# Kernel tuning notes

Hardware: AMD Instinct MI355X
Metric: run time of the kernel (lower is better)

Reference implementation:

```python
import jax, jax.numpy as jnp
import numpy as np

G, B, S, D = 4, 1, 1024, 2048   # num_gpus (chunks), batch, seq_local, model dim
H, DH = 32, 64                  # heads, dim_head; inner_dim = H*DH = D
EPS = 1e-6
NEG = -1e30                     # finite stand-in for -inf lse init (grad-safe)


def setup_inputs() -> dict:
    key = jax.random.key(0)
    ks = jax.random.split(key, 8)
    wsc = 1.0 / np.sqrt(D)  # keep pre-softmax logits in a sane range
    return {
        'x':  jax.random.normal(ks[0], (G, B, S, D), jnp.float32),
        'Wq': jax.random.normal(ks[1], (D, D), jnp.float32) * wsc,
        'bq': jnp.zeros((D,), jnp.float32),
        'Wk': jax.random.normal(ks[2], (D, D), jnp.float32) * wsc,
        'bk': jnp.zeros((D,), jnp.float32),
        'Wv': jax.random.normal(ks[3], (D, D), jnp.float32) * wsc,
        'bv': jnp.zeros((D,), jnp.float32),
        'qn_w': jnp.ones((D,), jnp.float32),
        'kn_w': jnp.ones((D,), jnp.float32),
        'Wo': jax.random.normal(ks[4], (D, D), jnp.float32) * wsc,
        'bo': jnp.zeros((D,), jnp.float32),
    }


def _rms_norm(t, w):
    return t * jax.lax.rsqrt(jnp.mean(t * t, axis=-1, keepdims=True) + EPS) * w


def reference(x, Wq, bq, Wk, bk, Wv, bv, qn_w, kn_w, Wo, bo):
    # x: [G, B, S, D] -- per-'GPU' sequence chunks
    q = _rms_norm(x @ Wq.T + bq, qn_w)
    k = _rms_norm(x @ Wk.T + bk, kn_w)
    v = x @ Wv.T + bv
    split = lambda t: t.reshape(G, B, S, H, DH).transpose(0, 1, 3, 2, 4)  # [G,B,H,S,DH]
    q, k, v = split(q), split(k), split(v)
    scale = 1.0 / np.sqrt(DH)

    out = jnp.zeros_like(q)
    lse = jnp.full((G, B, H, S, 1), NEG, q.dtype)
    kc, vc = k, v
    # Ring: each chunk attends to the visiting K/V chunk with online softmax.
    for _ in range(G):
        scores = jnp.einsum('gbhqd,gbhkd->gbhqk', q, kc) * scale
        m = scores.max(axis=-1, keepdims=True)
        e = jnp.exp(scores - m)
        ssum = e.sum(axis=-1, keepdims=True)
        chunk_lse = m + jnp.log(ssum)
        chunk_out = jnp.einsum('gbhqk,gbhkd->gbhqd', e / ssum, vc)
        new_lse = jnp.logaddexp(lse, chunk_lse)
        out = out * jnp.exp(lse - new_lse) + chunk_out * jnp.exp(chunk_lse - new_lse)
        lse = new_lse
        # rotate K/V around the ring: device i receives from device i-1
        kc = jnp.roll(kc, 1, axis=0)
        vc = jnp.roll(vc, 1, axis=0)

    o = out.transpose(0, 1, 3, 2, 4).reshape(G, B, S, H * DH)
    return o @ Wo.T + bo
```

## Files before the change

### kernel.cpp

```cpp
#include <hip/hip_runtime.h>

typedef __bf16 bf16x8 __attribute__((ext_vector_type(8)));
typedef float f32x4 __attribute__((ext_vector_type(4)));
typedef float f32x16 __attribute__((ext_vector_type(16)));
typedef unsigned short u16x8 __attribute__((ext_vector_type(8)));
typedef unsigned u32x2 __attribute__((ext_vector_type(2)));
typedef unsigned u32x4 __attribute__((ext_vector_type(4)));

__device__ __forceinline__ unsigned short f2bf(float f) {
  union { float f; unsigned u; } v; v.f = f;
  unsigned r = (v.u + 0x7fffu + ((v.u >> 16) & 1u)) >> 16;
  return (unsigned short)r;
}
__device__ __forceinline__ float bf2f(unsigned short s) {
  union { unsigned u; float f; } v; v.u = ((unsigned)s) << 16;
  return v.f;
}

#define GLD16(g, l)                                                        \
  __builtin_amdgcn_global_load_lds(                                        \
      (const __attribute__((address_space(1))) void*)(g),                  \
      (__attribute__((address_space(3))) void*)(l), 16, 0, 0)

__device__ __forceinline__ int swzc(int row, int colel) {
  return colel ^ ((((row & 7) ^ ((row >> 3) & 7)) & 7) << 3);
}

__device__ __forceinline__ u32x2 plswap(unsigned a, unsigned b) {
  return __builtin_amdgcn_permlane32_swap(a, b, false, false);
}
__device__ __forceinline__ float pair_sum(float x) {
  u32x2 r = plswap(__float_as_uint(x), __float_as_uint(x));
  return __uint_as_float(r.x) + __uint_as_float(r.y);
}
__device__ __forceinline__ unsigned cvtpk(float a, float b) {
  unsigned r;
  asm("v_cvt_pk_bf16_f32 %0, %1, %2" : "=v"(r) : "v"(a), "v"(b));
  return r;
}

__global__ __launch_bounds__(256) void cast_all_kernel(
    const float* __restrict__ x,
    const float* __restrict__ w0, const float* __restrict__ w1,
    const float* __restrict__ w2, const float* __restrict__ w3,
    unsigned short* __restrict__ xo,
    unsigned short* __restrict__ o0, unsigned short* __restrict__ o1,
    unsigned short* __restrict__ o2, unsigned short* __restrict__ o3) {
  int i = blockIdx.x * 256 + threadIdx.x;
  int stride = gridDim.x * 256;
  for (; i < 6291456; i += stride) {
    const float* src;
    unsigned short* dst;
    int j;
    if (i < 2097152) {
      src = x; dst = xo; j = i;
    } else {
      int k = i - 2097152;
      int sel = k >> 20;
      src = sel == 0 ? w0 : sel == 1 ? w1 : sel == 2 ? w2 : w3;
      dst = sel == 0 ? o0 : sel == 1 ? o1 : sel == 2 ? o2 : o3;
      j = k & 1048575;
    }
    float4 f = reinterpret_cast<const float4*>(src)[j];
    ushort4 s;
    s.x = f2bf(f.x); s.y = f2bf(f.y); s.z = f2bf(f.z); s.w = f2bf(f.w);
    reinterpret_cast<ushort4*>(dst)[j] = s;
  }
}


#define STG_A(STEP, KS, BUF)                                                   \
  GLD16(Ag + (size_t)(row0 + st_row0) * 2048 + (STEP) * 64 + (KS) * 32 +       \
            st_col0,                                                           \
        &ls[((BUF) * 2 + (KS)) * 4096 + (wid * 2) * 512]);                     \
  GLD16(Ag + (size_t)(row0 + st_row1) * 2048 + (STEP) * 64 + (KS) * 32 +       \
            st_col1,                                                           \
        &ls[((BUF) * 2 + (KS)) * 4096 + (wid * 2 + 1) * 512]);

#define STG_B(STEP, KS, BUF)                                                   \
  GLD16(Bg + (size_t)(col0 + st_row0) * 2048 + (STEP) * 64 + (KS) * 32 +       \
            st_col0,                                                           \
        &ls[16384 + ((BUF) * 2 + (KS)) * 4096 + (wid * 2) * 512]);             \
  GLD16(Bg + (size_t)(col0 + st_row1) * 2048 + (STEP) * 64 + (KS) * 32 +       \
            st_col1,                                                           \
        &ls[16384 + ((BUF) * 2 + (KS)) * 4096 + (wid * 2 + 1) * 512]);

#define VM8 asm volatile("s_waitcnt vmcnt(8)" ::: "memory");
#define VM4 asm volatile("s_waitcnt vmcnt(4)" ::: "memory");
#define VM0 asm volatile("s_waitcnt vmcnt(0)" ::: "memory");

#define PHASE4(BUF, KS, STG, VMW)                                              \
  {                                                                            \
    const int pb = ((BUF) * 2 + (KS)) * 4096;                                  \
    bf16x8 af0 = *(const bf16x8*)&ls[pb + offA[0]];                            \
    bf16x8 af1 = *(const bf16x8*)&ls[pb + offA[1]];                            \
    bf16x8 af2 = *(const bf16x8*)&ls[pb + offA[2]];                            \
    bf16x8 af3 = *(const bf16x8*)&ls[pb + offA[3]];                            \
    bf16x8 bf0 = *(const bf16x8*)&ls[16384 + pb + offB[0]];                    \
    bf16x8 bf1 = *(const bf16x8*)&ls[16384 + pb + offB[1]];                    \
    bf16x8 bf2 = *(const bf16x8*)&ls[16384 + pb + offB[2]];                    \
    bf16x8 bf3 = *(const bf16x8*)&ls[16384 + pb + offB[3]];                    \
    STG;                                                                       \
    __builtin_amdgcn_s_barrier();                                              \
    __builtin_amdgcn_s_setprio(1);                                             \
    acc[0][0] = __builtin_amdgcn_mfma_f32_16x16x32_bf16(af0, bf0, acc[0][0], 0, 0, 0); \
    acc[0][1] = __builtin_amdgcn_mfma_f32_16x16x32_bf16(af0, bf1, acc[0][1], 0, 0, 0); \
    acc[0][2] = __builtin_amdgcn_mfma_f32_16x16x32_bf16(af0, bf2, acc[0][2], 0, 0, 0); \
    acc[0][3] = __builtin_amdgcn_mfma_f32_16x16x32_bf16(af0, bf3, acc[0][3], 0, 0, 0); \
    acc[1][0] = __builtin_amdgcn_mfma_f32_16x16x32_bf16(af1, bf0, acc[1][0], 0, 0, 0); \
    acc[1][1] = __builtin_amdgcn_mfma_f32_16x16x32_bf16(af1, bf1, acc[1][1], 0, 0, 0); \
    acc[1][2] = __builtin_amdgcn_mfma_f32_16x16x32_bf16(af1, bf2, acc[1][2], 0, 0, 0); \
    acc[1][3] = __builtin_amdgcn_mfma_f32_16x16x32_bf16(af1, bf3, acc[1][3], 0, 0, 0); \
    acc[2][0] = __builtin_amdgcn_mfma_f32_16x16x32_bf16(af2, bf0, acc[2][0], 0, 0, 0); \
    acc[2][1] = __builtin_amdgcn_mfma_f32_16x16x32_bf16(af2, bf1, acc[2][1], 0, 0, 0); \
    acc[2][2] = __builtin_amdgcn_mfma_f32_16x16x32_bf16(af2, bf2, acc[2][2], 0, 0, 0); \
    acc[2][3] = __builtin_amdgcn_mfma_f32_16x16x32_bf16(af2, bf3, acc[2][3], 0, 0, 0); \
    acc[3][0] = __builtin_amdgcn_mfma_f32_16x16x32_bf16(af3, bf0, acc[3][0], 0, 0, 0); \
    acc[3][1] = __builtin_amdgcn_mfma_f32_16x16x32_bf16(af3, bf1, acc[3][1], 0, 0, 0); \
    acc[3][2] = __builtin_amdgcn_mfma_f32_16x16x32_bf16(af3, bf2, acc[3][2], 0, 0, 0); \
    acc[3][3] = __builtin_amdgcn_mfma_f32_16x16x32_bf16(af3, bf3, acc[3][3], 0, 0, 0); \
    __builtin_amdgcn_s_setprio(0);                                             \
    VMW;                                                                       \
    __builtin_amdgcn_s_barrier();                                              \
  }

template <int F32OUT>
__global__ __launch_bounds__(256, 2) void gemm4p(
    const unsigned short* __restrict__ Ag,
    const unsigned short* __restrict__ W0, const unsigned short* __restrict__ W1,
    const unsigned short* __restrict__ W2,
    const float* __restrict__ b0, const float* __restrict__ b1,
    const float* __restrict__ b2,
    void* __restrict__ C0, void* __restrict__ C1, void* __restrict__ C2) {
  extern __shared__ __align__(16) unsigned short ls[];

  const int lin = blockIdx.y * gridDim.x + blockIdx.x;
  const int cpx = (gridDim.x * gridDim.y) >> 3;
  const int swz = (lin & 7) * cpx + (lin >> 3);
  const int bx = swz % gridDim.x, by = swz / gridDim.x;

  const int gcol = bx * 128;
  const int sel = gcol >> 11;
  const unsigned short* Bg = sel == 0 ? W0 : sel == 1 ? W1 : W2;
  const float* bias = sel == 0 ? b0 : sel == 1 ? b1 : b2;
  void* Cp = sel == 0 ? C0 : sel == 1 ? C1 : C2;
  const int col0 = gcol & 2047;
  const int row0 = by * 128;

  const int tid = threadIdx.x, lane = tid & 63, wid = tid >> 6;
  const int l15 = lane & 15, l4 = lane >> 4;
  const int wm = wid >> 1, wn = wid & 1;

  const int ci0 = wid * 2, ci1 = wid * 2 + 1;
  const int st_row0 = ci0 * 16 + (lane >> 2);
  const int st_row1 = ci1 * 16 + (lane >> 2);
  const int sl2a = ((lane >> 2) & 3) ^ ((lane >> 4) & 3);
  const int st_col0 = (((lane & 3) ^ (sl2a ^ (ci0 & 3))) * 8);
  const int st_col1 = (((lane & 3) ^ (sl2a ^ (ci1 & 3))) * 8);

  const int lsel = (l15 & 3) ^ ((l15 >> 2) & 3);
  int offA[4], offB[4];
#pragma unroll
  for (int f = 0; f < 4; ++f)
    offA[f] = (wm * 64 + f * 16 + l15) * 32 + ((l4 ^ lsel ^ (f & 3)) & 3) * 8;
#pragma unroll
  for (int ni = 0; ni < 4; ++ni)
    offB[ni] =
        (wn * 64 + ni * 16 + l15) * 32 + ((l4 ^ lsel ^ ((wn * 4 + ni) & 3)) & 3) * 8;

  f32x4 acc[4][4] = {};

  STG_A(0, 0, 0); STG_B(0, 0, 0);
  STG_A(0, 1, 0); STG_B(0, 1, 0);
  STG_A(1, 0, 1); STG_B(1, 0, 1);
  VM8;
  __builtin_amdgcn_s_barrier();

  for (int it = 0; it < 15; ++it) {
    const int sE = 2 * it, sO = sE + 1;
    PHASE4(0, 0, STG_A(sO, 1, 1) STG_B(sO, 1, 1), VM8);
    PHASE4(0, 1, STG_A(sE + 2, 0, 0) STG_B(sE + 2, 0, 0), VM8);
    PHASE4(1, 0, STG_A(sE + 2, 1, 0) STG_B(sE + 2, 1, 0), VM8);
    PHASE4(1, 1, STG_A(sO + 2, 0, 1) STG_B(sO + 2, 0, 1), VM8);
  }
  PHASE4(0, 0, STG_A(31, 1, 1) STG_B(31, 1, 1), VM8);
  PHASE4(0, 1, , VM4);
  PHASE4(1, 0, , VM0);
  PHASE4(1, 1, , );

#pragma unroll
  for (int f = 0; f < 4; ++f)
#pragma unroll
    for (int ni = 0; ni < 4; ++ni)
#pragma unroll
      for (int r = 0; r < 4; ++r) {
        int row = row0 + wm * 64 + f * 16 + l4 * 4 + r;
        int col = col0 + wn * 64 + ni * 16 + l15;
        float v = acc[f][ni][r] + bias[col];
        if (F32OUT)
          ((float*)Cp)[(size_t)row * 2048 + col] = v;
        else
          ((unsigned short*)Cp)[(size_t)row * 2048 + col] = f2bf(v);
      }
}

__global__ __launch_bounds__(256) void rmsnorm2_kernel(
    unsigned short* __restrict__ Qb, unsigned short* __restrict__ Kb,
    const float* __restrict__ qw, const float* __restrict__ kw) {
  const int row = blockIdx.x;
  unsigned short* p;
  const float* w;
  if (row < 4096) { p = Qb + (size_t)row * 2048; w = qw; }
  else            { p = Kb + (size_t)(row - 4096) * 2048; w = kw; }
  const int tid = threadIdx.x;
  u16x8 v = *(const u16x8*)&p[tid * 8];
  float f[8];
  float ss = 0.f;
#pragma unroll
  for (int j = 0; j < 8; ++j) { f[j] = bf2f(v[j]); ss += f[j] * f[j]; }
#pragma unroll
  for (int m = 1; m < 64; m <<= 1) ss += __shfl_xor(ss, m, 64);
  __shared__ float red[4];
  const int wid = tid >> 6, lane = tid & 63;
  if (lane == 0) red[wid] = ss;
  __syncthreads();
  float tot = red[0] + red[1] + red[2] + red[3];
  float rs = rsqrtf(tot * (1.0f / 2048.0f) + 1e-6f);
  u16x8 o;
#pragma unroll
  for (int j = 0; j < 8; ++j) o[j] = f2bf(f[j] * rs * w[tid * 8 + j]);
  *(u16x8*)&p[tid * 8] = o;
}

__global__ __launch_bounds__(256, 2) void flash_attn(
    const unsigned short* __restrict__ Q, const unsigned short* __restrict__ K,
    const unsigned short* __restrict__ V, unsigned short* __restrict__ O) {
  __shared__ unsigned short Ks[2][64 * 64];
  __shared__ unsigned short Vs[2][64 * 64];
  const int bid = blockIdx.x;
  const int sw = (bid & 7) * 64 + (bid >> 3);
  const int h = sw >> 4;
  const int q0 = (sw & 15) * 256;
  const int tid = threadIdx.x, lane = tid & 63, wid = tid >> 6;
  const int l31 = lane & 31, hi = lane >> 5;

  const int kr0 = wid * 16 + (lane >> 3);
  const int kc0 = (lane & 7) * 8;
  const int vkey = (tid & 31) * 2;
  const int vd0 = (tid >> 5) * 8;

  const float QSCALE = 0.125f * 1.44269504f;
  bf16x8 qf0[4], qf1[4];
  {
    const int qr0 = q0 + wid * 64 + l31;
#pragma unroll
    for (int kt = 0; kt < 4; ++kt) {
      bf16x8 r0 = *(const bf16x8*)&Q[(size_t)qr0 * 2048 + h * 64 + kt * 16 + hi * 8];
      bf16x8 r1 = *(const bf16x8*)&Q[(size_t)(qr0 + 32) * 2048 + h * 64 + kt * 16 + hi * 8];
#pragma unroll
      for (int j = 0; j < 8; ++j) {
        qf0[kt][j] = (__bf16)((float)r0[j] * QSCALE);
        qf1[kt][j] = (__bf16)((float)r1[j] * QSCALE);
      }
    }
  }

  int off[2][4];
#pragma unroll
  for (int kb = 0; kb < 2; ++kb) {
    const int row = kb * 32 + l31;
    const int sl = (((row & 7) ^ ((row >> 3) & 7)) & 7) << 3;
#pragma unroll
    for (int kt = 0; kt < 4; ++kt)
      off[kb][kt] = row * 64 + ((kt * 16 + hi * 8) ^ sl);
  }

  float l0 = 0.f, l1 = 0.f;
  f32x16 oa0[2] = {}, oa1[2] = {};

  u16x8 kreg0, kreg1, vreg0, vreg1;
  auto loadKV = [&](int kt0) {
    kreg0 = *(const u16x8*)&K[(size_t)(kt0 + kr0) * 2048 + h * 64 + kc0];
    kreg1 = *(const u16x8*)&K[(size_t)(kt0 + kr0 + 8) * 2048 + h * 64 + kc0];
    vreg0 = *(const u16x8*)&V[(size_t)(kt0 + vkey) * 2048 + h * 64 + vd0];
    vreg1 = *(const u16x8*)&V[(size_t)(kt0 + vkey + 1) * 2048 + h * 64 + vd0];
  };
  auto writeKV = [&](int b) {
    *(u16x8*)&Ks[b][kr0 * 64 + swzc(kr0, kc0)] = kreg0;
    *(u16x8*)&Ks[b][(kr0 + 8) * 64 + swzc(kr0 + 8, kc0)] = kreg1;
#pragma unroll
    for (int d = 0; d < 8; ++d) {
      int row = vd0 + d;
      *(unsigned*)&Vs[b][row * 64 + swzc(row, vkey)] =
          (unsigned)vreg0[d] | ((unsigned)vreg1[d] << 16);
    }
  };

  loadKV(0);
  writeKV(0);
  __syncthreads();

  for (int t = 0; t < 64; ++t) {
    const int cur = t & 1;
    if (t < 63) loadKV((t + 1) * 64);

    const unsigned short* Kc = Ks[cur];
    const unsigned short* Vc = Vs[cur];

    bf16x8 kf[2][4];
#pragma unroll
    for (int kb = 0; kb < 2; ++kb)
#pragma unroll
      for (int kt = 0; kt < 4; ++kt)
        kf[kb][kt] = *(const bf16x8*)&Kc[off[kb][kt]];

    f32x16 st0[2], st1[2];
    __builtin_amdgcn_s_setprio(1);
#pragma unroll
    for (int kb = 0; kb < 2; ++kb) {
      f32x16 a = {};
#pragma unroll
      for (int kt = 0; kt < 4; ++kt)
        a = __builtin_amdgcn_mfma_f32_32x32x16_bf16(kf[kb][kt], qf0[kt], a, 0, 0, 0);
      st0[kb] = a;
    }
#pragma unroll
    for (int kb = 0; kb < 2; ++kb) {
      f32x16 a = {};
#pragma unroll
      for (int kt = 0; kt < 4; ++kt)
        a = __builtin_amdgcn_mfma_f32_32x32x16_bf16(kf[kb][kt], qf1[kt], a, 0, 0, 0);
      st1[kb] = a;
    }
    __builtin_amdgcn_s_setprio(0);

    unsigned pk0[16], pk1[16];
    {
      float s0 = 0.f, s1 = 0.f, s2 = 0.f, s3 = 0.f;
#pragma unroll
      for (int kb = 0; kb < 2; ++kb)
#pragma unroll
        for (int j = 0; j < 8; ++j) {
          float pa = __builtin_amdgcn_exp2f(st0[kb][2 * j]);
          float pb = __builtin_amdgcn_exp2f(st0[kb][2 * j + 1]);
          if ((j & 3) == 0) s0 += pa + pb;
          else if ((j & 3) == 1) s1 += pa + pb;
          else if ((j & 3) == 2) s2 += pa + pb;
          else s3 += pa + pb;
          pk0[kb * 8 + j] = cvtpk(pa, pb);
        }
      l0 += (s0 + s1) + (s2 + s3);
    }
    {
      float s0 = 0.f, s1 = 0.f, s2 = 0.f, s3 = 0.f;
#pragma unroll
      for (int kb = 0; kb < 2; ++kb)
#pragma unroll
        for (int j = 0; j < 8; ++j) {
          float pa = __builtin_amdgcn_exp2f(st1[kb][2 * j]);
          float pb = __builtin_amdgcn_exp2f(st1[kb][2 * j + 1]);
          if ((j & 3) == 0) s0 += pa + pb;
          else if ((j & 3) == 1) s1 += pa + pb;
          else if ((j & 3) == 2) s2 += pa + pb;
          else s3 += pa + pb;
          pk1[kb * 8 + j] = cvtpk(pa, pb);
        }
      l1 += (s0 + s1) + (s2 + s3);
    }

    bf16x8 pfrag0[4], pfrag1[4];
#pragma unroll
    for (int kt = 0; kt < 4; ++kt) {
      u32x2 sa = plswap(pk0[4 * kt + 0], pk0[4 * kt + 2]);
      u32x2 sb = plswap(pk0[4 * kt + 1], pk0[4 * kt + 3]);
      union { u32x4 u; bf16x8 b; } w;
      w.u.x = sa.x; w.u.y = sb.x; w.u.z = sa.y; w.u.w = sb.y;
      pfrag0[kt] = w.b;
      u32x2 sc = plswap(pk1[4 * kt + 0], pk1[4 * kt + 2]);
      u32x2 sd = plswap(pk1[4 * kt + 1], pk1[4 * kt + 3]);
      union { u32x4 u; bf16x8 b; } w2;
      w2.u.x = sc.x; w2.u.y = sd.x; w2.u.z = sc.y; w2.u.w = sd.y;
      pfrag1[kt] = w2.b;
    }

    __builtin_amdgcn_s_setprio(1);
#pragma unroll
    for (int dv = 0; dv < 2; ++dv) {
      bf16x8 vf[4];
#pragma unroll
      for (int kt = 0; kt < 4; ++kt)
        vf[kt] = *(const bf16x8*)&Vc[off[dv][kt]];
#pragma unroll
      for (int kt = 0; kt < 4; ++kt)
        oa0[dv] = __builtin_amdgcn_mfma_f32_32x32x16_bf16(vf[kt], pfrag0[kt], oa0[dv], 0, 0, 0);
#pragma unroll
      for (int kt = 0; kt < 4; ++kt)
        oa1[dv] = __builtin_amdgcn_mfma_f32_32x32x16_bf16(vf[kt], pfrag1[kt], oa1[dv], 0, 0, 0);
    }
    __builtin_amdgcn_s_setprio(0);

    if (t < 63) {
      writeKV(cur ^ 1);
      __syncthreads();
    }
  }

  const float inv0 = 1.0f / pair_sum(l0);
  const float inv1 = 1.0f / pair_sum(l1);
  const int qr0 = q0 + wid * 64 + l31;
#pragma unroll
  for (int dv = 0; dv < 2; ++dv)
#pragma unroll
    for (int tq = 0; tq < 4; ++tq) {
      int dh = 32 * dv + 8 * tq + 4 * hi;
      unsigned a0 = cvtpk(oa0[dv][4 * tq + 0] * inv0, oa0[dv][4 * tq + 1] * inv0);
      unsigned a1 = cvtpk(oa0[dv][4 * tq + 2] * inv0, oa0[dv][4 * tq + 3] * inv0);
      u32x2 wa = {a0, a1};
      *(u32x2*)&O[(size_t)qr0 * 2048 + h * 64 + dh] = wa;
      unsigned b0 = cvtpk(oa1[dv][4 * tq + 0] * inv1, oa1[dv][4 * tq + 1] * inv1);
      unsigned b1 = cvtpk(oa1[dv][4 * tq + 2] * inv1, oa1[dv][4 * tq + 3] * inv1);
      u32x2 wb = {b0, b1};
      *(u32x2*)&O[(size_t)(qr0 + 32) * 2048 + h * 64 + dh] = wb;
    }
}

extern "C" void kernel_launch(void* const* d_in, const int* in_sizes, int n_in,
                              void* d_out, int out_size, void* d_ws, size_t ws_size,
                              hipStream_t stream) {
  const float* x  = (const float*)d_in[0];
  const float* Wq = (const float*)d_in[1];
  const float* bq = (const float*)d_in[2];
  const float* Wk = (const float*)d_in[3];
  const float* bk = (const float*)d_in[4];
  const float* Wv = (const float*)d_in[5];
  const float* bv = (const float*)d_in[6];
  const float* qn = (const float*)d_in[7];
  const float* kn = (const float*)d_in[8];
  const float* Wo = (const float*)d_in[9];
  const float* bo = (const float*)d_in[10];

  char* w = (char*)d_ws;
  unsigned short* Xbf = (unsigned short*)(w);
  unsigned short* Wqb = (unsigned short*)(w + 16777216);
  unsigned short* Wkb = (unsigned short*)(w + 25165824);
  unsigned short* Wvb = (unsigned short*)(w + 33554432);
  unsigned short* Wob = (unsigned short*)(w + 41943040);
  unsigned short* Qb  = (unsigned short*)(w + 50331648);
  unsigned short* Kb  = (unsigned short*)(w + 67108864);
  unsigned short* Vb  = (unsigned short*)(w + 83886080);
  unsigned short* Ob  = Xbf;

  cast_all_kernel<<<3072, 256, 0, stream>>>(x, Wq, Wk, Wv, Wo,
                                            Xbf, Wqb, Wkb, Wvb, Wob);

  gemm4p<0><<<dim3(48, 32), 256, 65536, stream>>>(
      Xbf, Wqb, Wkb, Wvb, bq, bk, bv, Qb, Kb, Vb);

  rmsnorm2_kernel<<<8192, 256, 0, stream>>>(Qb, Kb, qn, kn);

  flash_attn<<<512, 256, 0, stream>>>(Qb, Kb, Vb, Ob);

  gemm4p<1><<<dim3(16, 32), 256, 65536, stream>>>(
      Ob, Wob, Wob, Wob, bo, bo, bo, d_out, d_out, d_out);
}
```

Before: 362.4 us.

## Enlarge GEMM tile to 256x128 with 512 threads and 4-stage K pipeline

```diff
diff --git a/kernel.cpp b/kernel.cpp
--- a/kernel.cpp
+++ b/kernel.cpp
@@ -69,70 +69,64 @@
 }
 
 
-#define STG_A(STEP, KS, BUF)                                                   \
-  GLD16(Ag + (size_t)(row0 + st_row0) * 2048 + (STEP) * 64 + (KS) * 32 +       \
-            st_col0,                                                           \
-        &ls[((BUF) * 2 + (KS)) * 4096 + (wid * 2) * 512]);                     \
-  GLD16(Ag + (size_t)(row0 + st_row1) * 2048 + (STEP) * 64 + (KS) * 32 +       \
-            st_col1,                                                           \
-        &ls[((BUF) * 2 + (KS)) * 4096 + (wid * 2 + 1) * 512]);
-
-#define STG_B(STEP, KS, BUF)                                                   \
-  GLD16(Bg + (size_t)(col0 + st_row0) * 2048 + (STEP) * 64 + (KS) * 32 +       \
-            st_col0,                                                           \
-        &ls[16384 + ((BUF) * 2 + (KS)) * 4096 + (wid * 2) * 512]);             \
-  GLD16(Bg + (size_t)(col0 + st_row1) * 2048 + (STEP) * 64 + (KS) * 32 +       \
-            st_col1,                                                           \
-        &ls[16384 + ((BUF) * 2 + (KS)) * 4096 + (wid * 2 + 1) * 512]);
-
-#define VM8 asm volatile("s_waitcnt vmcnt(8)" ::: "memory");
-#define VM4 asm volatile("s_waitcnt vmcnt(4)" ::: "memory");
+#define SGA(SLICE, SLOT)                                                       \
+  GLD16(Ag + (size_t)(row0 + ar0) * 2048 + (SLICE) * 32 + ac0,                 \
+        &As[SLOT][ci0 * 512]);                                                 \
+  GLD16(Ag + (size_t)(row0 + ar1) * 2048 + (SLICE) * 32 + ac1,                 \
+        &As[SLOT][ci1 * 512]);
+
+#define SGB(SLICE, SLOT)                                                       \
+  GLD16(Bg + (size_t)(col0 + br0) * 2048 + (SLICE) * 32 + bc0,                 \
+        &Bs[SLOT][wid * 512]);
+
+#define VM6 asm volatile("s_waitcnt vmcnt(6)" ::: "memory");
+#define VM3 asm volatile("s_waitcnt vmcnt(3)" ::: "memory");
 #define VM0 asm volatile("s_waitcnt vmcnt(0)" ::: "memory");
 
-#define PHASE4(BUF, KS, STG, VMW)                                              \
+#define PH256(SLOT, STG, VMW)                                                  \
   {                                                                            \
-    const int pb = ((BUF) * 2 + (KS)) * 4096;                                  \
-    bf16x8 af0 = *(const bf16x8*)&ls[pb + offA[0]];                            \
-    bf16x8 af1 = *(const bf16x8*)&ls[pb + offA[1]];                            \
-    bf16x8 af2 = *(const bf16x8*)&ls[pb + offA[2]];                            \
-    bf16x8 af3 = *(const bf16x8*)&ls[pb + offA[3]];                            \
-    bf16x8 bf0 = *(const bf16x8*)&ls[16384 + pb + offB[0]];                    \
-    bf16x8 bf1 = *(const bf16x8*)&ls[16384 + pb + offB[1]];                    \
-    bf16x8 bf2 = *(const bf16x8*)&ls[16384 + pb + offB[2]];                    \
-    bf16x8 bf3 = *(const bf16x8*)&ls[16384 + pb + offB[3]];                    \
+    bf16x8 a0 = *(const bf16x8*)&As[SLOT][offA[0]];                            \
+    bf16x8 a1 = *(const bf16x8*)&As[SLOT][offA[1]];                            \
+    bf16x8 a2 = *(const bf16x8*)&As[SLOT][offA[2]];                            \
+    bf16x8 a3 = *(const bf16x8*)&As[SLOT][offA[3]];                            \
+    bf16x8 b0 = *(const bf16x8*)&Bs[SLOT][offB[0]];                            \
+    bf16x8 b1 = *(const bf16x8*)&Bs[SLOT][offB[1]];                            \
+    bf16x8 b2 = *(const bf16x8*)&Bs[SLOT][offB[2]];                            \
+    bf16x8 b3 = *(const bf16x8*)&Bs[SLOT][offB[3]];                            \
     STG;                                                                       \
     __builtin_amdgcn_s_barrier();                                              \
     __builtin_amdgcn_s_setprio(1);                                             \
-    acc[0][0] = __builtin_amdgcn_mfma_f32_16x16x32_bf16(af0, bf0, acc[0][0], 0, 0, 0); \
-    acc[0][1] = __builtin_amdgcn_mfma_f32_16x16x32_bf16(af0, bf1, acc[0][1], 0, 0, 0); \
-    acc[0][2] = __builtin_amdgcn_mfma_f32_16x16x32_bf16(af0, bf2, acc[0][2], 0, 0, 0); \
-    acc[0][3] = __builtin_amdgcn_mfma_f32_16x16x32_bf16(af0, bf3, acc[0][3], 0, 0, 0); \
-    acc[1][0] = __builtin_amdgcn_mfma_f32_16x16x32_bf16(af1, bf0, acc[1][0], 0, 0, 0); \
-    acc[1][1] = __builtin_amdgcn_mfma_f32_16x16x32_bf16(af1, bf1, acc[1][1], 0, 0, 0); \
-    acc[1][2] = __builtin_amdgcn_mfma_f32_16x16x32_bf16(af1, bf2, acc[1][2], 0, 0, 0); \
-    acc[1][3] = __builtin_amdgcn_mfma_f32_16x16x32_bf16(af1, bf3, acc[1][3], 0, 0, 0); \
-    acc[2][0] = __builtin_amdgcn_mfma_f32_16x16x32_bf16(af2, bf0, acc[2][0], 0, 0, 0); \
-    acc[2][1] = __builtin_amdgcn_mfma_f32_16x16x32_bf16(af2, bf1, acc[2][1], 0, 0, 0); \
-    acc[2][2] = __builtin_amdgcn_mfma_f32_16x16x32_bf16(af2, bf2, acc[2][2], 0, 0, 0); \
-    acc[2][3] = __builtin_amdgcn_mfma_f32_16x16x32_bf16(af2, bf3, acc[2][3], 0, 0, 0); \
-    acc[3][0] = __builtin_amdgcn_mfma_f32_16x16x32_bf16(af3, bf0, acc[3][0], 0, 0, 0); \
-    acc[3][1] = __builtin_amdgcn_mfma_f32_16x16x32_bf16(af3, bf1, acc[3][1], 0, 0, 0); \
-    acc[3][2] = __builtin_amdgcn_mfma_f32_16x16x32_bf16(af3, bf2, acc[3][2], 0, 0, 0); \
-    acc[3][3] = __builtin_amdgcn_mfma_f32_16x16x32_bf16(af3, bf3, acc[3][3], 0, 0, 0); \
+    acc[0][0] = __builtin_amdgcn_mfma_f32_16x16x32_bf16(a0, b0, acc[0][0], 0, 0, 0); \
+    acc[0][1] = __builtin_amdgcn_mfma_f32_16x16x32_bf16(a0, b1, acc[0][1], 0, 0, 0); \
+    acc[0][2] = __builtin_amdgcn_mfma_f32_16x16x32_bf16(a0, b2, acc[0][2], 0, 0, 0); \
+    acc[0][3] = __builtin_amdgcn_mfma_f32_16x16x32_bf16(a0, b3, acc[0][3], 0, 0, 0); \
+    acc[1][0] = __builtin_amdgcn_mfma_f32_16x16x32_bf16(a1, b0, acc[1][0], 0, 0, 0); \
+    acc[1][1] = __builtin_amdgcn_mfma_f32_16x16x32_bf16(a1, b1, acc[1][1], 0, 0, 0); \
+    acc[1][2] = __builtin_amdgcn_mfma_f32_16x16x32_bf16(a1, b2, acc[1][2], 0, 0, 0); \
+    acc[1][3] = __builtin_amdgcn_mfma_f32_16x16x32_bf16(a1, b3, acc[1][3], 0, 0, 0); \
+    acc[2][0] = __builtin_amdgcn_mfma_f32_16x16x32_bf16(a2, b0, acc[2][0], 0, 0, 0); \
+    acc[2][1] = __builtin_amdgcn_mfma_f32_16x16x32_bf16(a2, b1, acc[2][1], 0, 0, 0); \
+    acc[2][2] = __builtin_amdgcn_mfma_f32_16x16x32_bf16(a2, b2, acc[2][2], 0, 0, 0); \
+    acc[2][3] = __builtin_amdgcn_mfma_f32_16x16x32_bf16(a2, b3, acc[2][3], 0, 0, 0); \
+    acc[3][0] = __builtin_amdgcn_mfma_f32_16x16x32_bf16(a3, b0, acc[3][0], 0, 0, 0); \
+    acc[3][1] = __builtin_amdgcn_mfma_f32_16x16x32_bf16(a3, b1, acc[3][1], 0, 0, 0); \
+    acc[3][2] = __builtin_amdgcn_mfma_f32_16x16x32_bf16(a3, b2, acc[3][2], 0, 0, 0); \
+    acc[3][3] = __builtin_amdgcn_mfma_f32_16x16x32_bf16(a3, b3, acc[3][3], 0, 0, 0); \
     __builtin_amdgcn_s_setprio(0);                                             \
     VMW;                                                                       \
     __builtin_amdgcn_s_barrier();                                              \
   }
 
 template <int F32OUT>
-__global__ __launch_bounds__(256, 2) void gemm4p(
+__global__ __launch_bounds__(512, 2) void gemm256(
     const unsigned short* __restrict__ Ag,
     const unsigned short* __restrict__ W0, const unsigned short* __restrict__ W1,
     const unsigned short* __restrict__ W2,
     const float* __restrict__ b0, const float* __restrict__ b1,
     const float* __restrict__ b2,
     void* __restrict__ C0, void* __restrict__ C1, void* __restrict__ C2) {
-  extern __shared__ __align__(16) unsigned short ls[];
+  __shared__ unsigned short As[4][8192];
+  __shared__ unsigned short Bs[4][4096];
 
   const int lin = blockIdx.y * gridDim.x + blockIdx.x;
   const int cpx = (gridDim.x * gridDim.y) >> 3;
@@ -145,48 +139,49 @@
   const float* bias = sel == 0 ? b0 : sel == 1 ? b1 : b2;
   void* Cp = sel == 0 ? C0 : sel == 1 ? C1 : C2;
   const int col0 = gcol & 2047;
-  const int row0 = by * 128;
+  const int row0 = by * 256;
 
   const int tid = threadIdx.x, lane = tid & 63, wid = tid >> 6;
   const int l15 = lane & 15, l4 = lane >> 4;
   const int wm = wid >> 1, wn = wid & 1;
 
+  const int sl2a = ((lane >> 2) & 3) ^ ((lane >> 4) & 3);
   const int ci0 = wid * 2, ci1 = wid * 2 + 1;
-  const int st_row0 = ci0 * 16 + (lane >> 2);
-  const int st_row1 = ci1 * 16 + (lane >> 2);
-  const int sl2a = ((lane >> 2) & 3) ^ ((lane >> 4) & 3);
-  const int st_col0 = (((lane & 3) ^ (sl2a ^ (ci0 & 3))) * 8);
-  const int st_col1 = (((lane & 3) ^ (sl2a ^ (ci1 & 3))) * 8);
+  const int ar0 = ci0 * 16 + (lane >> 2);
+  const int ar1 = ci1 * 16 + (lane >> 2);
+  const int ac0 = (((lane & 3) ^ sl2a ^ (ci0 & 3)) & 3) * 8;
+  const int ac1 = (((lane & 3) ^ sl2a ^ (ci1 & 3)) & 3) * 8;
+  const int br0 = wid * 16 + (lane >> 2);
+  const int bc0 = (((lane & 3) ^ sl2a ^ (wid & 3)) & 3) * 8;
 
   const int lsel = (l15 & 3) ^ ((l15 >> 2) & 3);
   int offA[4], offB[4];
 #pragma unroll
   for (int f = 0; f < 4; ++f)
-    offA[f] = (wm * 64 + f * 16 + l15) * 32 + ((l4 ^ lsel ^ (f & 3)) & 3) * 8;
+    offA[f] = (wm * 64 + f * 16 + l15) * 32 + ((l4 ^ lsel ^ f) & 3) * 8;
 #pragma unroll
   for (int ni = 0; ni < 4; ++ni)
-    offB[ni] =
-        (wn * 64 + ni * 16 + l15) * 32 + ((l4 ^ lsel ^ ((wn * 4 + ni) & 3)) & 3) * 8;
+    offB[ni] = (wn * 64 + ni * 16 + l15) * 32 + ((l4 ^ lsel ^ ni) & 3) * 8;
 
   f32x4 acc[4][4] = {};
 
-  STG_A(0, 0, 0); STG_B(0, 0, 0);
-  STG_A(0, 1, 0); STG_B(0, 1, 0);
-  STG_A(1, 0, 1); STG_B(1, 0, 1);
-  VM8;
+  SGA(0, 0); SGB(0, 0);
+  SGA(1, 1); SGB(1, 1);
+  SGA(2, 2); SGB(2, 2);
+  VM6;
   __builtin_amdgcn_s_barrier();
 
   for (int it = 0; it < 15; ++it) {
-    const int sE = 2 * it, sO = sE + 1;
-    PHASE4(0, 0, STG_A(sO, 1, 1) STG_B(sO, 1, 1), VM8);
-    PHASE4(0, 1, STG_A(sE + 2, 0, 0) STG_B(sE + 2, 0, 0), VM8);
-    PHASE4(1, 0, STG_A(sE + 2, 1, 0) STG_B(sE + 2, 1, 0), VM8);
-    PHASE4(1, 1, STG_A(sO + 2, 0, 1) STG_B(sO + 2, 0, 1), VM8);
-  }
-  PHASE4(0, 0, STG_A(31, 1, 1) STG_B(31, 1, 1), VM8);
-  PHASE4(0, 1, , VM4);
-  PHASE4(1, 0, , VM0);
-  PHASE4(1, 1, , );
+    const int s = 4 * it;
+    PH256(0, SGA(s + 3, 3) SGB(s + 3, 3), VM6);
+    PH256(1, SGA(s + 4, 0) SGB(s + 4, 0), VM6);
+    PH256(2, SGA(s + 5, 1) SGB(s + 5, 1), VM6);
+    PH256(3, SGA(s + 6, 2) SGB(s + 6, 2), VM6);
+  }
+  PH256(0, SGA(63, 3) SGB(63, 3), VM6);
+  PH256(1, , VM3);
+  PH256(2, , VM0);
+  PH256(3, , );
 
 #pragma unroll
   for (int f = 0; f < 4; ++f)
@@ -453,13 +448,13 @@
   cast_all_kernel<<<3072, 256, 0, stream>>>(x, Wq, Wk, Wv, Wo,
                                             Xbf, Wqb, Wkb, Wvb, Wob);
 
-  gemm4p<0><<<dim3(48, 32), 256, 65536, stream>>>(
+  gemm256<0><<<dim3(48, 16), 512, 0, stream>>>(
       Xbf, Wqb, Wkb, Wvb, bq, bk, bv, Qb, Kb, Vb);
 
   rmsnorm2_kernel<<<8192, 256, 0, stream>>>(Qb, Kb, qn, kn);
 
   flash_attn<<<512, 256, 0, stream>>>(Qb, Kb, Vb, Ob);
 
-  gemm4p<1><<<dim3(16, 32), 256, 65536, stream>>>(
+  gemm256<1><<<dim3(16, 16), 512, 0, stream>>>(
       Ob, Wob, Wob, Wob, bo, bo, bo, d_out, d_out, d_out);
 }
```

Measured after the change: 357.8 us. Within noise of the previous version (-1.3%).
